# Kernel optimization log

Measured on AMD Instinct MI355X. Metric: run time of the kernel, lower is better.

The kernel has to match this reference:

```python
import jax, jax.numpy as jnp
import numpy as np

B, N, D = 1, 128, 64
H, DH = 8, 64            # heads, per-head dim; dim_inner = dim*dim_head = 512
DI = H * DH              # 512
L = 2                    # max_degree
S = 1 + 2 * L            # 5 degree slots: (h, r_1..L, x_1..L)
MLP = 1024               # int(2.0 * dim_inner)
EPS = 1e-5


def _ln(x, g):
    m = x.mean(-1, keepdims=True)
    v = ((x - m) ** 2).mean(-1, keepdims=True)
    return (x - m) * jax.lax.rsqrt(v + EPS) * g


def setup_inputs() -> dict:
    key = jax.random.key(0)
    ks = jax.random.split(key, 16)
    rn = lambda k, s, sc=1.0: jax.random.normal(k, s, dtype=jnp.float32) * sc
    return {
        "h": rn(ks[0], (B, N, D)),
        "t_ij": rn(ks[1], (B, N, N, D)),
        "r1": rn(ks[2], (B, N, N, 3)),
        "r2": rn(ks[3], (B, N, N, 5)),
        "x1": rn(ks[4], (B, N, D, 3)),
        "x2": rn(ks[5], (B, N, D, 5)),
        "g_hi": jnp.ones((D,), jnp.float32),
        "g_hj": jnp.ones((D,), jnp.float32),
        "Wq": rn(ks[6], (D, DI), D ** -0.5),
        "Wk": rn(ks[7], (D, DI), D ** -0.5),
        "Wv1": rn(ks[8], (D, MLP), D ** -0.5),
        "bv1": jnp.zeros((MLP,), jnp.float32),
        "Wv2": rn(ks[9], (MLP, S * DI), MLP ** -0.5),
        "bv2": jnp.zeros((S * DI,), jnp.float32),
        "Wp1": rn(ks[10], (D, MLP), D ** -0.5),
        "bp1": jnp.zeros((MLP,), jnp.float32),
        "Wp2": rn(ks[11], (MLP, S * DI), MLP ** -0.5),
        "bp2": jnp.zeros((S * DI,), jnp.float32),
        "Wev": rn(ks[12], (D, S * DI), D ** -0.5),
        "Wc": rn(ks[13], (DI, D), DI ** -0.5),
    }


def reference(h, t_ij, r1, r2, x1, x2, g_hi, g_hj, Wq, Wk, Wv1, bv1, Wv2, bv2,
              Wp1, bp1, Wp2, bp2, Wev, Wc):
    b, n, d = h.shape
    hi, hj = _ln(h, g_hi), _ln(h, g_hj)
    q = (hi @ Wq).reshape(b, n, H, DH).transpose(0, 2, 1, 3)                # b h i d
    k = (hj @ Wk).reshape(b, n, H, DH).transpose(0, 2, 1, 3)                # b h j d
    vals = (jax.nn.silu(hj @ Wv1 + bv1) @ Wv2 + bv2)
    vals = vals.reshape(b, n, S, H, DH).transpose(0, 3, 1, 2, 4)            # b h j s d
    pav = (jax.nn.silu(hj @ Wp1 + bp1) @ Wp2 + bp2)
    pav = pav.reshape(b, n, S, H, DH).transpose(0, 3, 1, 2, 4)              # b h j s d
    # NOTE: source uses to_edge_values for BOTH edge keys and edge values (to_edge_keys is dead code)
    ev = (t_ij @ Wev).reshape(b, n, n, S, H, DH).transpose(0, 4, 1, 2, 3, 5)  # b h i j s d
    sim_num = jnp.einsum('bhid,bhjd->bhij', q, k)                           # b h i j
    sim_den = jnp.einsum('bhid,bhijsd->bhis', q, ev)                        # b h i s
    attn = sim_num[..., None] / sim_den[:, :, :, None, :]                   # b h i j s (quotient attention)
    sea = attn[..., None] * vals[:, :, None] + ev * pav[:, :, None]         # b h i j s d
    out = sea.transpose(0, 2, 3, 4, 1, 5).reshape(b, n, n, S, DI) @ Wc      # b i j s D
    # split sizes (1, L, L) along the s axis: h scale, r_ij scales, x scales
    h_new = h + out[:, :, :, 0, :].sum(axis=2)                              # sum over neighbors j
    xs, rs = (x1, x2), (r1, r2)
    x_new = [jnp.einsum('bjdm,bijd->bidm', xs[l], out[:, :, :, 1 + L + l, :])
             + jnp.einsum('bijm,bijd->bidm', rs[l], out[:, :, :, 1 + l, :])
             for l in range(L)]
    return (h_new, x_new[0], x_new[1])
```

## Files before the change

### kernel.cpp

```cpp
#include <hip/hip_runtime.h>
#include <hip/hip_bf16.h>

typedef __hip_bfloat16 bf16;
typedef __attribute__((ext_vector_type(8))) short short8;
typedef __attribute__((ext_vector_type(4))) float f32x4;

#define NN 128
#define DD_ 64
#define HH_ 8
#define DH_ 64
#define DI_ 512
#define SS_ 5
#define MLPD 1024
#define SDI 2560

__device__ __forceinline__ float wave_sum64(float v) {
#pragma unroll
    for (int off = 32; off > 0; off >>= 1) v += __shfl_xor(v, off, 64);
    return v;
}

__device__ __forceinline__ unsigned short f2bf_u(float f) {
    unsigned u = __float_as_uint(f);
    u += 0x7FFF + ((u >> 16) & 1);
    return (unsigned short)(u >> 16);
}
__device__ __forceinline__ float bfu2f(unsigned short s) {
    return __uint_as_float(((unsigned)s) << 16);
}
__device__ __forceinline__ unsigned pk2(unsigned short a, unsigned short b) {
    return (unsigned)a | ((unsigned)b << 16);
}

__global__ __launch_bounds__(256) void k_front(
    const float* __restrict__ h, const float* __restrict__ ghi, const float* __restrict__ ghj,
    const float* __restrict__ Wq, const float* __restrict__ Wk,
    const float* __restrict__ Wv1, const float* __restrict__ bv1,
    const float* __restrict__ Wp1, const float* __restrict__ bp1,
    float* __restrict__ q, float* __restrict__ k,
    float* __restrict__ a1, float* __restrict__ p1) {
    int i = blockIdx.x, ch = blockIdx.y, t = threadIdx.x;
    int d = t & 63;
    __shared__ float hib[DD_], hjb[DD_];
    float x = h[i * DD_ + d];
    float s = wave_sum64(x);
    float s2 = wave_sum64(x * x);
    float m = s * (1.0f / DD_);
    float v = s2 * (1.0f / DD_) - m * m;
    float r = rsqrtf(v + 1e-5f);
    float xc = (x - m) * r;
    if (t < 64) { hib[d] = xc * ghi[d]; hjb[d] = xc * ghj[d]; }
    __syncthreads();
    {
        int c = ch * 128 + (t & 127);
        const float* W = (t < 128) ? Wq : Wk;
        const float* hb = (t < 128) ? hib : hjb;
        float a = 0.f;
#pragma unroll 8
        for (int dd = 0; dd < DD_; dd++) a += hb[dd] * W[dd * DI_ + c];
        float* dstqk = (t < 128) ? q : k;
        dstqk[i * DI_ + c] = a;
    }
    {
        int c = ch * 256 + t;
        float av = 0.f, ap = 0.f;
#pragma unroll 4
        for (int dd = 0; dd < DD_; dd++) {
            float hv = hjb[dd];
            av += hv * Wv1[dd * MLPD + c];
            ap += hv * Wp1[dd * MLPD + c];
        }
        float xv = av + bv1[c], xp = ap + bp1[c];
        a1[i * MLPD + c] = xv / (1.0f + expf(-xv));
        p1[i * MLPD + c] = xp / (1.0f + expf(-xp));
    }
}

#define KSP 8
#define KSL 128
__global__ __launch_bounds__(256) void k_mlp2(const float* __restrict__ a1,
                                              const float* __restrict__ p1,
                                              const float* __restrict__ Wv2,
                                              const float* __restrict__ Wp2,
                                              float* __restrict__ part) {
    int ct = blockIdx.x, ks = blockIdx.y, t = threadIdx.x;
    int c0 = ct * 128;
    bool isp = c0 >= 2560;
    int c0l = c0 - (isp ? 2560 : 0);
    const float* __restrict__ src = isp ? p1 : a1;
    const float* __restrict__ W = isp ? Wp2 : Wv2;
    int k0base = ks * KSL;
    __shared__ float As[128][33];
    __shared__ float Ws[32][128];
    int tc = t & 7;
    int tj = t >> 3;
    int j0 = tj * 4;
    float acc[4][16];
#pragma unroll
    for (int jj = 0; jj < 4; jj++)
#pragma unroll
        for (int cc = 0; cc < 16; cc++) acc[jj][cc] = 0.f;
    for (int kc = 0; kc < KSL; kc += 32) {
        int k0 = k0base + kc;
        __syncthreads();
#pragma unroll
        for (int it = 0; it < 4; it++) {
            int slot = t + it * 256;
            int jj = slot >> 3, f4 = (slot & 7) * 4;
            float4 v = *(const float4*)&src[jj * MLPD + k0 + f4];
            As[jj][f4 + 0] = v.x; As[jj][f4 + 1] = v.y;
            As[jj][f4 + 2] = v.z; As[jj][f4 + 3] = v.w;
        }
#pragma unroll
        for (int it = 0; it < 4; it++) {
            int slot = t + it * 256;
            int kk = slot >> 5, f4 = (slot & 31) * 4;
            float4 v = *(const float4*)&W[(size_t)(k0 + kk) * SDI + c0l + f4];
            *(float4*)&Ws[kk][f4] = v;
        }
        __syncthreads();
#pragma unroll 4
        for (int kx = 0; kx < 32; kx++) {
            float a[4];
#pragma unroll
            for (int jj = 0; jj < 4; jj++) a[jj] = As[j0 + jj][kx];
#pragma unroll
            for (int cf = 0; cf < 4; cf++) {
                float4 wv = *(const float4*)&Ws[kx][tc * 4 + cf * 32];
#pragma unroll
                for (int jj = 0; jj < 4; jj++) {
                    acc[jj][cf * 4 + 0] += a[jj] * wv.x;
                    acc[jj][cf * 4 + 1] += a[jj] * wv.y;
                    acc[jj][cf * 4 + 2] += a[jj] * wv.z;
                    acc[jj][cf * 4 + 3] += a[jj] * wv.w;
                }
            }
        }
    }
#pragma unroll
    for (int jj = 0; jj < 4; jj++)
#pragma unroll
        for (int cf = 0; cf < 4; cf++) {
            float4 v = make_float4(acc[jj][cf * 4 + 0], acc[jj][cf * 4 + 1],
                                   acc[jj][cf * 4 + 2], acc[jj][cf * 4 + 3]);
            *(float4*)&part[(size_t)ks * 655360 + (size_t)(j0 + jj) * 5120 + c0 + tc * 4 + cf * 32] = v;
        }
}

__global__ __launch_bounds__(512) void k_post(const float* __restrict__ part,
                                              const float* __restrict__ bv2,
                                              const float* __restrict__ bp2,
                                              const float* __restrict__ Wc,
                                              float* __restrict__ pav,
                                              float* __restrict__ VC) {
    int j = blockIdx.x, y = blockIdx.y, t = threadIdx.x;
    if (y < 5) {
        int s = y;
        __shared__ float vlds[512];
        int e = s * 512 + t;
        float sum = 0.f;
#pragma unroll
        for (int p = 0; p < KSP; p++) sum += part[(size_t)p * 655360 + (size_t)j * 5120 + e];
        vlds[t] = sum + bv2[e];
        __syncthreads();
        int dd = t & 63;
        int hbase = t - dd;
        float acc = 0.f;
#pragma unroll 8
        for (int d2 = 0; d2 < DH_; d2++) acc += vlds[hbase + d2] * Wc[(size_t)(hbase + d2) * DD_ + dd];
        VC[(size_t)(j * SS_ + s) * DI_ + t] = acc;
    } else {
        int s = y - 5;
        int e = 2560 + s * 512 + t;
        float sum = 0.f;
#pragma unroll
        for (int p = 0; p < KSP; p++) sum += part[(size_t)p * 655360 + (size_t)j * 5120 + e];
        pav[(size_t)j * SDI + s * 512 + t] = sum + bp2[s * 512 + t];
    }
}

__global__ __launch_bounds__(640) void k_den(const float* __restrict__ tij,
                                             const float* __restrict__ Wev,
                                             const float* __restrict__ q,
                                             float* __restrict__ rsd) {
    int i = blockIdx.x, half = blockIdx.y, t = threadIdx.x;
    __shared__ float red[10][64];
    __shared__ float Tl[64];
    __shared__ float ql[DI_];
    int c = t & 63, jw = t >> 6;
    float s = 0.f;
    for (int j = jw; j < NN; j += 10) s += tij[(size_t)(i * NN + j) * DD_ + c];
    red[jw][c] = s;
    if (t < DI_) ql[t] = q[i * DI_ + t];
    __syncthreads();
    if (t < 64) {
        float a = 0.f;
#pragma unroll
        for (int r2 = 0; r2 < 10; r2++) a += red[r2][t];
        Tl[t] = a;
    }
    __syncthreads();
#pragma unroll
    for (int kx = 0; kx < 2; kx++) {
        int u = half * 1280 + kx * 640 + t;
        float ev = 0.f;
#pragma unroll 8
        for (int cc = 0; cc < DD_; cc++) ev += Tl[cc] * Wev[(size_t)cc * SDI + u];
        float den = wave_sum64(ev * ql[u & 511]);
        if ((t & 63) == 0) {
            int g = u >> 6;
            int ss = g >> 3, hh = g & 7;
            rsd[i * 40 + hh * SS_ + ss] = 1.0f / den;
        }
    }
}

__global__ __launch_bounds__(512) void k_simnum(const float* __restrict__ q,
                                                const float* __restrict__ k,
                                                float* __restrict__ sn) {
    int i = blockIdx.x, yh = blockIdx.y, t = threadIdx.x;
    int hh = yh * 4 + (t >> 7), j = t & 127;
    __shared__ float qb[256];
    if (t < 256) qb[t] = q[i * DI_ + yh * 256 + t];
    __syncthreads();
    float a = 0.f;
    const float* kr = &k[(size_t)j * DI_ + hh * DH_];
    const float* qr = &qb[(hh - yh * 4) * DH_];
#pragma unroll 8
    for (int d = 0; d < DH_; d++) a += qr[d] * kr[d];
    sn[i * 1024 + hh * NN + j] = a;
}

#define KCM 64
__global__ __launch_bounds__(256) void k_M(const float* __restrict__ pav,
                                           const float* __restrict__ Wev,
                                           const float* __restrict__ Wc,
                                           float* __restrict__ M) {
    int j = blockIdx.x, s = blockIdx.y, t = threadIdx.x;
    int lane = t & 63, w = t >> 6;
    __shared__ float P[DI_];
    __shared__ unsigned short Ahi[64][72], Alo[64][72];
    __shared__ unsigned short Bhi[64][72], Blo[64][72];
    P[t] = pav[j * SDI + s * DI_ + t];
    P[t + 256] = pav[j * SDI + s * DI_ + t + 256];
    f32x4 acc[4];
#pragma unroll
    for (int n = 0; n < 4; n++) acc[n] = (f32x4){0.f, 0.f, 0.f, 0.f};
    __syncthreads();
    for (int u0 = 0; u0 < DI_; u0 += KCM) {
        {
            int c = t >> 2, ug = (t & 3) * 16;
            const float* wevp = &Wev[(size_t)c * SDI + s * DI_ + u0 + ug];
            unsigned short ah[16], al[16];
#pragma unroll
            for (int e = 0; e < 16; e += 4) {
                float4 wv = *(const float4*)(wevp + e);
                float4 pv = *(const float4*)&P[u0 + ug + e];
                float av[4] = {wv.x * pv.x, wv.y * pv.y, wv.z * pv.z, wv.w * pv.w};
#pragma unroll
                for (int z = 0; z < 4; z++) {
                    unsigned short hh2 = f2bf_u(av[z]);
                    ah[e + z] = hh2;
                    al[e + z] = f2bf_u(av[z] - bfu2f(hh2));
                }
            }
            *(uint4*)&Ahi[c][ug] = make_uint4(pk2(ah[0], ah[1]), pk2(ah[2], ah[3]),
                                              pk2(ah[4], ah[5]), pk2(ah[6], ah[7]));
            *(uint4*)&Ahi[c][ug + 8] = make_uint4(pk2(ah[8], ah[9]), pk2(ah[10], ah[11]),
                                                  pk2(ah[12], ah[13]), pk2(ah[14], ah[15]));
            *(uint4*)&Alo[c][ug] = make_uint4(pk2(al[0], al[1]), pk2(al[2], al[3]),
                                              pk2(al[4], al[5]), pk2(al[6], al[7]));
            *(uint4*)&Alo[c][ug + 8] = make_uint4(pk2(al[8], al[9]), pk2(al[10], al[11]),
                                                  pk2(al[12], al[13]), pk2(al[14], al[15]));
        }
        {
            int dd = t & 63, ub = (t >> 6) * 16;
            unsigned short bh[16], bl[16];
#pragma unroll
            for (int e = 0; e < 16; e++) {
                float v = Wc[(size_t)(u0 + ub + e) * DD_ + dd];
                unsigned short hh2 = f2bf_u(v);
                bh[e] = hh2;
                bl[e] = f2bf_u(v - bfu2f(hh2));
            }
            *(uint4*)&Bhi[dd][ub] = make_uint4(pk2(bh[0], bh[1]), pk2(bh[2], bh[3]),
                                               pk2(bh[4], bh[5]), pk2(bh[6], bh[7]));
            *(uint4*)&Bhi[dd][ub + 8] = make_uint4(pk2(bh[8], bh[9]), pk2(bh[10], bh[11]),
                                                   pk2(bh[12], bh[13]), pk2(bh[14], bh[15]));
            *(uint4*)&Blo[dd][ub] = make_uint4(pk2(bl[0], bl[1]), pk2(bl[2], bl[3]),
                                               pk2(bl[4], bl[5]), pk2(bl[6], bl[7]));
            *(uint4*)&Blo[dd][ub + 8] = make_uint4(pk2(bl[8], bl[9]), pk2(bl[10], bl[11]),
                                                   pk2(bl[12], bl[13]), pk2(bl[14], bl[15]));
        }
        __syncthreads();
#pragma unroll
        for (int kk = 0; kk < 2; kk++) {
            int ko = kk * 32 + (lane >> 4) * 8;
            short8 a_h = *(const short8*)&Ahi[w * 16 + (lane & 15)][ko];
            short8 a_l = *(const short8*)&Alo[w * 16 + (lane & 15)][ko];
#pragma unroll
            for (int n = 0; n < 4; n++) {
                short8 b_h = *(const short8*)&Bhi[n * 16 + (lane & 15)][ko];
                short8 b_l = *(const short8*)&Blo[n * 16 + (lane & 15)][ko];
                acc[n] = __builtin_amdgcn_mfma_f32_16x16x32_bf16(a_h, b_h, acc[n], 0, 0, 0);
                acc[n] = __builtin_amdgcn_mfma_f32_16x16x32_bf16(a_h, b_l, acc[n], 0, 0, 0);
                acc[n] = __builtin_amdgcn_mfma_f32_16x16x32_bf16(a_l, b_h, acc[n], 0, 0, 0);
            }
        }
        __syncthreads();
    }
    float* Mp = &M[(size_t)(j * SS_ + s) * 4096];
#pragma unroll
    for (int n = 0; n < 4; n++)
#pragma unroll
        for (int r = 0; r < 4; r++) {
            int c = w * 16 + (lane >> 4) * 4 + r;
            int dd = n * 16 + (lane & 15);
            Mp[c * 64 + dd] = acc[n][r];
        }
}

__global__ __launch_bounds__(256) void k_out(const float* __restrict__ M, const float* __restrict__ VC,
                      const float* __restrict__ sn, const float* __restrict__ rsd,
                      const float* __restrict__ tij, float* __restrict__ outb) {
    int j = blockIdx.x, s = blockIdx.y, ic = blockIdx.z, t = threadIdx.x;
    int il = t >> 6, dd = t & 63;
    __shared__ float VCl[DI_];
    __shared__ float tl[4][64];
    __shared__ float snl[4][8];
    __shared__ float rl[4][8];
    float Mcol[64];
    const float* Mp = &M[(size_t)(j * SS_ + s) * 4096];
#pragma unroll
    for (int c = 0; c < 64; c++) Mcol[c] = Mp[c * 64 + dd];
    VCl[t] = VC[(j * SS_ + s) * DI_ + t];
    VCl[t + 256] = VC[(j * SS_ + s) * DI_ + t + 256];
    __syncthreads();
    for (int ib = ic * 64; ib < ic * 64 + 64; ib += 4) {
        int i = ib + il;
        tl[il][dd] = tij[(size_t)(i * NN + j) * DD_ + dd];
        if (dd < 8) {
            snl[il][dd] = sn[i * 1024 + dd * NN + j];
            rl[il][dd] = rsd[i * 40 + dd * SS_ + s];
        }
        float A = 0.f;
#pragma unroll
        for (int hh = 0; hh < HH_; hh++) A += snl[il][hh] * rl[il][hh] * VCl[hh * DH_ + dd];
        float E = 0.f;
        const float4* tl4 = (const float4*)&tl[il][0];
#pragma unroll
        for (int c4 = 0; c4 < 16; c4++) {
            float4 tv = tl4[c4];
            E += tv.x * Mcol[4 * c4] + tv.y * Mcol[4 * c4 + 1] +
                 tv.z * Mcol[4 * c4 + 2] + tv.w * Mcol[4 * c4 + 3];
        }
        outb[((size_t)(i * NN + j) * SS_ + s) * 64 + dd] = A + E;
    }
}

#define JC 16
#define JPC 8
__global__ void k_red1(const float* __restrict__ outb,
                       const float* __restrict__ r1, const float* __restrict__ r2,
                       const float* __restrict__ x1, const float* __restrict__ x2,
                       float* __restrict__ pr) {
    int i = blockIdx.x, jc = blockIdx.y, t = threadIdx.x;
    int s = t >> 6, dd = t & 63;
    int jbeg = jc * JPC;
    float hacc = 0.f;
    float am[5] = {0.f, 0.f, 0.f, 0.f, 0.f};
    for (int jj = 0; jj < JPC; jj++) {
        int j = jbeg + jj;
        float ov = outb[((size_t)(i * NN + j) * SS_ + s) * 64 + dd];
        if (s == 0) {
            hacc += ov;
        } else if (s == 1) {
#pragma unroll
            for (int m = 0; m < 3; m++) am[m] += r1[(i * NN + j) * 3 + m] * ov;
        } else if (s == 2) {
#pragma unroll
            for (int m = 0; m < 5; m++) am[m] += r2[(i * NN + j) * 5 + m] * ov;
        } else if (s == 3) {
#pragma unroll
            for (int m = 0; m < 3; m++) am[m] += x1[(j * DD_ + dd) * 3 + m] * ov;
        } else {
#pragma unroll
            for (int m = 0; m < 5; m++) am[m] += x2[(j * DD_ + dd) * 5 + m] * ov;
        }
    }
    float* rec = &pr[(size_t)(i * JC + jc) * 1088];
    if (s == 0) {
        rec[dd] = hacc;
    } else if (s == 1) {
#pragma unroll
        for (int m = 0; m < 3; m++) rec[64 + dd * 3 + m] = am[m];
    } else if (s == 2) {
#pragma unroll
        for (int m = 0; m < 5; m++) rec[256 + dd * 5 + m] = am[m];
    } else if (s == 3) {
#pragma unroll
        for (int m = 0; m < 3; m++) rec[576 + dd * 3 + m] = am[m];
    } else {
#pragma unroll
        for (int m = 0; m < 5; m++) rec[768 + dd * 5 + m] = am[m];
    }
}

__global__ void k_red2(const float* __restrict__ pr, const float* __restrict__ h,
                       float* __restrict__ dst) {
    int i = blockIdx.x, t = threadIdx.x;
    int s = t >> 6, dd = t & 63;
    const float* base = &pr[(size_t)i * JC * 1088];
    if (s == 0) {
        float v = 0.f;
#pragma unroll
        for (int c = 0; c < JC; c++) v += base[c * 1088 + dd];
        dst[i * DD_ + dd] = h[i * DD_ + dd] + v;
    } else if (s == 3) {
        float v[3] = {0.f, 0.f, 0.f};
#pragma unroll
        for (int c = 0; c < JC; c++) {
#pragma unroll
            for (int m = 0; m < 3; m++)
                v[m] += base[c * 1088 + 64 + dd * 3 + m] + base[c * 1088 + 576 + dd * 3 + m];
        }
#pragma unroll
        for (int m = 0; m < 3; m++)
            dst[8192 + (i * DD_ + dd) * 3 + m] = v[m];
    } else if (s == 4) {
        float v[5] = {0.f, 0.f, 0.f, 0.f, 0.f};
#pragma unroll
        for (int c = 0; c < JC; c++) {
#pragma unroll
            for (int m = 0; m < 5; m++)
                v[m] += base[c * 1088 + 256 + dd * 5 + m] + base[c * 1088 + 768 + dd * 5 + m];
        }
#pragma unroll
        for (int m = 0; m < 5; m++)
            dst[8192 + 24576 + (i * DD_ + dd) * 5 + m] = v[m];
    }
}

extern "C" void kernel_launch(void* const* d_in, const int* in_sizes, int n_in,
                              void* d_out, int out_size, void* d_ws, size_t ws_size,
                              hipStream_t stream) {
    const float* h_in = (const float*)d_in[0];
    const float* tij = (const float*)d_in[1];
    const float* r1 = (const float*)d_in[2];
    const float* r2 = (const float*)d_in[3];
    const float* x1 = (const float*)d_in[4];
    const float* x2 = (const float*)d_in[5];
    const float* ghi = (const float*)d_in[6];
    const float* ghj = (const float*)d_in[7];
    const float* Wq = (const float*)d_in[8];
    const float* Wk = (const float*)d_in[9];
    const float* Wv1 = (const float*)d_in[10];
    const float* bv1 = (const float*)d_in[11];
    const float* Wv2 = (const float*)d_in[12];
    const float* bv2 = (const float*)d_in[13];
    const float* Wp1 = (const float*)d_in[14];
    const float* bp1 = (const float*)d_in[15];
    const float* Wp2 = (const float*)d_in[16];
    const float* bp2 = (const float*)d_in[17];
    const float* Wev = (const float*)d_in[18];
    const float* Wc = (const float*)d_in[19];
    float* dst = (float*)d_out;

    float* w = (float*)d_ws;
    size_t off = 16;
    auto alloc = [&](size_t n) { float* p = w + off; off += n; return p; };
    float* q    = alloc(65536);
    float* k    = alloc(65536);
    float* a1   = alloc(131072);
    float* p1   = alloc(131072);
    float* pav  = alloc(327680);
    float* VC   = alloc(327680);
    float* sn   = alloc(131072);
    float* rsd  = alloc(5120);
    float* M    = alloc(2621440);
    float* outb = alloc(5242880);
    float* part = alloc(5242880);
    float* pr   = alloc(2228224);

    k_front<<<dim3(128, 4), dim3(256), 0, stream>>>(h_in, ghi, ghj, Wq, Wk, Wv1, bv1, Wp1, bp1,
                                                    q, k, a1, p1);
    k_mlp2<<<dim3(40, KSP), dim3(256), 0, stream>>>(a1, p1, Wv2, Wp2, part);
    k_post<<<dim3(128, 10), dim3(512), 0, stream>>>(part, bv2, bp2, Wc, pav, VC);
    k_den<<<dim3(128, 2), dim3(640), 0, stream>>>(tij, Wev, q, rsd);
    k_simnum<<<dim3(128, 2), dim3(512), 0, stream>>>(q, k, sn);
    k_M<<<dim3(128, 5), dim3(256), 0, stream>>>(pav, Wev, Wc, M);
    k_out<<<dim3(128, 5, 2), dim3(256), 0, stream>>>(M, VC, sn, rsd, tij, outb);
    k_red1<<<dim3(128, JC), dim3(320), 0, stream>>>(outb, r1, r2, x1, x2, pr);
    k_red2<<<dim3(128), dim3(320), 0, stream>>>(pr, h_in, dst);
}
```

Measured before the change: 244.4 us.

## Move MLP2 and k_out GEMMs onto split-bf16 MFMA

Rewrites k_mlp2 to use bf16 hi/lo split MFMA (three products per tile) instead of scalar FP32 FMAs. The tile changes to 64 columns and the K split to 4, which halves the partial buffer. k_out becomes a 128x64 MFMA GEMM per (j,s) block: the sn·rsd·VC term is folded in as a zero-padded K=8 chunk and the tij·M product as two K=32 chunks. This removes scalar FMA throughput limits, at the cost of converting to bf16 pairs on the fly and dropping the low×low product, which loses a little accuracy.

```diff
diff --git a/kernel.cpp b/kernel.cpp
--- a/kernel.cpp
+++ b/kernel.cpp
@@ -76,75 +76,98 @@
     }
 }
 
-#define KSP 8
-#define KSL 128
+#define KS2 4
 __global__ __launch_bounds__(256) void k_mlp2(const float* __restrict__ a1,
                                               const float* __restrict__ p1,
                                               const float* __restrict__ Wv2,
                                               const float* __restrict__ Wp2,
                                               float* __restrict__ part) {
     int ct = blockIdx.x, ks = blockIdx.y, t = threadIdx.x;
-    int c0 = ct * 128;
+    int c0 = ct * 64;
     bool isp = c0 >= 2560;
     int c0l = c0 - (isp ? 2560 : 0);
     const float* __restrict__ src = isp ? p1 : a1;
     const float* __restrict__ W = isp ? Wp2 : Wv2;
-    int k0base = ks * KSL;
-    __shared__ float As[128][33];
-    __shared__ float Ws[32][128];
-    int tc = t & 7;
-    int tj = t >> 3;
-    int j0 = tj * 4;
-    float acc[4][16];
-#pragma unroll
-    for (int jj = 0; jj < 4; jj++)
-#pragma unroll
-        for (int cc = 0; cc < 16; cc++) acc[jj][cc] = 0.f;
-    for (int kc = 0; kc < KSL; kc += 32) {
-        int k0 = k0base + kc;
+    int kbase = ks * 256;
+    __shared__ unsigned short Ahi[128][40], Alo[128][40];
+    __shared__ unsigned short Bhi[64][40], Blo[64][40];
+    int lane = t & 63, wv = t >> 6;
+    int l15 = lane & 15, quad = lane >> 4;
+    f32x4 acc[2][4];
+#pragma unroll
+    for (int mt = 0; mt < 2; mt++)
+#pragma unroll
+        for (int nt = 0; nt < 4; nt++) acc[mt][nt] = (f32x4){0.f, 0.f, 0.f, 0.f};
+    int aj = t >> 1, ak = (t & 1) * 16;
+    int bc = t & 63, bk = (t >> 6) * 8;
+    for (int kc = 0; kc < 8; kc++) {
+        int k0 = kbase + kc * 32;
         __syncthreads();
-#pragma unroll
-        for (int it = 0; it < 4; it++) {
-            int slot = t + it * 256;
-            int jj = slot >> 3, f4 = (slot & 7) * 4;
-            float4 v = *(const float4*)&src[jj * MLPD + k0 + f4];
-            As[jj][f4 + 0] = v.x; As[jj][f4 + 1] = v.y;
-            As[jj][f4 + 2] = v.z; As[jj][f4 + 3] = v.w;
-        }
-#pragma unroll
-        for (int it = 0; it < 4; it++) {
-            int slot = t + it * 256;
-            int kk = slot >> 5, f4 = (slot & 31) * 4;
-            float4 v = *(const float4*)&W[(size_t)(k0 + kk) * SDI + c0l + f4];
-            *(float4*)&Ws[kk][f4] = v;
+        {
+            unsigned short h16[16], l16[16];
+            const float* ap = &src[(size_t)aj * MLPD + k0 + ak];
+#pragma unroll
+            for (int e = 0; e < 16; e += 4) {
+                float4 v = *(const float4*)(ap + e);
+                float vv[4] = {v.x, v.y, v.z, v.w};
+#pragma unroll
+                for (int z = 0; z < 4; z++) {
+                    unsigned short hb = f2bf_u(vv[z]);
+                    h16[e + z] = hb;
+                    l16[e + z] = f2bf_u(vv[z] - bfu2f(hb));
+                }
+            }
+            *(uint4*)&Ahi[aj][ak] = make_uint4(pk2(h16[0], h16[1]), pk2(h16[2], h16[3]),
+                                               pk2(h16[4], h16[5]), pk2(h16[6], h16[7]));
+            *(uint4*)&Ahi[aj][ak + 8] = make_uint4(pk2(h16[8], h16[9]), pk2(h16[10], h16[11]),
+                                                   pk2(h16[12], h16[13]), pk2(h16[14], h16[15]));
+            *(uint4*)&Alo[aj][ak] = make_uint4(pk2(l16[0], l16[1]), pk2(l16[2], l16[3]),
+                                               pk2(l16[4], l16[5]), pk2(l16[6], l16[7]));
+            *(uint4*)&Alo[aj][ak + 8] = make_uint4(pk2(l16[8], l16[9]), pk2(l16[10], l16[11]),
+                                                   pk2(l16[12], l16[13]), pk2(l16[14], l16[15]));
+        }
+        {
+            unsigned short h8[8], l8[8];
+#pragma unroll
+            for (int e = 0; e < 8; e++) {
+                float v = W[(size_t)(k0 + bk + e) * SDI + c0l + bc];
+                unsigned short hb = f2bf_u(v);
+                h8[e] = hb;
+                l8[e] = f2bf_u(v - bfu2f(hb));
+            }
+            *(uint4*)&Bhi[bc][bk] = make_uint4(pk2(h8[0], h8[1]), pk2(h8[2], h8[3]),
+                                               pk2(h8[4], h8[5]), pk2(h8[6], h8[7]));
+            *(uint4*)&Blo[bc][bk] = make_uint4(pk2(l8[0], l8[1]), pk2(l8[2], l8[3]),
+                                               pk2(l8[4], l8[5]), pk2(l8[6], l8[7]));
         }
         __syncthreads();
-#pragma unroll 4
-        for (int kx = 0; kx < 32; kx++) {
-            float a[4];
-#pragma unroll
-            for (int jj = 0; jj < 4; jj++) a[jj] = As[j0 + jj][kx];
-#pragma unroll
-            for (int cf = 0; cf < 4; cf++) {
-                float4 wv = *(const float4*)&Ws[kx][tc * 4 + cf * 32];
-#pragma unroll
-                for (int jj = 0; jj < 4; jj++) {
-                    acc[jj][cf * 4 + 0] += a[jj] * wv.x;
-                    acc[jj][cf * 4 + 1] += a[jj] * wv.y;
-                    acc[jj][cf * 4 + 2] += a[jj] * wv.z;
-                    acc[jj][cf * 4 + 3] += a[jj] * wv.w;
-                }
-            }
-        }
-    }
-#pragma unroll
-    for (int jj = 0; jj < 4; jj++)
-#pragma unroll
-        for (int cf = 0; cf < 4; cf++) {
-            float4 v = make_float4(acc[jj][cf * 4 + 0], acc[jj][cf * 4 + 1],
-                                   acc[jj][cf * 4 + 2], acc[jj][cf * 4 + 3]);
-            *(float4*)&part[(size_t)ks * 655360 + (size_t)(j0 + jj) * 5120 + c0 + tc * 4 + cf * 32] = v;
-        }
+        int ko = quad * 8;
+        short8 a_h0 = *(const short8*)&Ahi[(wv * 2 + 0) * 16 + l15][ko];
+        short8 a_l0 = *(const short8*)&Alo[(wv * 2 + 0) * 16 + l15][ko];
+        short8 a_h1 = *(const short8*)&Ahi[(wv * 2 + 1) * 16 + l15][ko];
+        short8 a_l1 = *(const short8*)&Alo[(wv * 2 + 1) * 16 + l15][ko];
+#pragma unroll
+        for (int nt = 0; nt < 4; nt++) {
+            short8 b_h = *(const short8*)&Bhi[nt * 16 + l15][ko];
+            short8 b_l = *(const short8*)&Blo[nt * 16 + l15][ko];
+            acc[0][nt] = __builtin_amdgcn_mfma_f32_16x16x32_bf16(a_h0, b_h, acc[0][nt], 0, 0, 0);
+            acc[0][nt] = __builtin_amdgcn_mfma_f32_16x16x32_bf16(a_h0, b_l, acc[0][nt], 0, 0, 0);
+            acc[0][nt] = __builtin_amdgcn_mfma_f32_16x16x32_bf16(a_l0, b_h, acc[0][nt], 0, 0, 0);
+            acc[1][nt] = __builtin_amdgcn_mfma_f32_16x16x32_bf16(a_h1, b_h, acc[1][nt], 0, 0, 0);
+            acc[1][nt] = __builtin_amdgcn_mfma_f32_16x16x32_bf16(a_h1, b_l, acc[1][nt], 0, 0, 0);
+            acc[1][nt] = __builtin_amdgcn_mfma_f32_16x16x32_bf16(a_l1, b_h, acc[1][nt], 0, 0, 0);
+        }
+    }
+#pragma unroll
+    for (int mt = 0; mt < 2; mt++)
+#pragma unroll
+        for (int nt = 0; nt < 4; nt++)
+#pragma unroll
+            for (int r = 0; r < 4; r++) {
+                int j = (wv * 2 + mt) * 16 + quad * 4 + r;
+                int cc = c0 + nt * 16 + l15;
+                part[(size_t)ks * 655360 + (size_t)j * 5120 + cc] = acc[mt][nt][r];
+            }
 }
 
 __global__ __launch_bounds__(512) void k_post(const float* __restrict__ part,
@@ -160,7 +183,7 @@
         int e = s * 512 + t;
         float sum = 0.f;
 #pragma unroll
-        for (int p = 0; p < KSP; p++) sum += part[(size_t)p * 655360 + (size_t)j * 5120 + e];
+        for (int p = 0; p < KS2; p++) sum += part[(size_t)p * 655360 + (size_t)j * 5120 + e];
         vlds[t] = sum + bv2[e];
         __syncthreads();
         int dd = t & 63;
@@ -174,7 +197,7 @@
         int e = 2560 + s * 512 + t;
         float sum = 0.f;
 #pragma unroll
-        for (int p = 0; p < KSP; p++) sum += part[(size_t)p * 655360 + (size_t)j * 5120 + e];
+        for (int p = 0; p < KS2; p++) sum += part[(size_t)p * 655360 + (size_t)j * 5120 + e];
         pav[(size_t)j * SDI + s * 512 + t] = sum + bp2[s * 512 + t];
     }
 }
@@ -321,41 +344,147 @@
 }
 
 __global__ __launch_bounds__(256) void k_out(const float* __restrict__ M, const float* __restrict__ VC,
-                      const float* __restrict__ sn, const float* __restrict__ rsd,
-                      const float* __restrict__ tij, float* __restrict__ outb) {
-    int j = blockIdx.x, s = blockIdx.y, ic = blockIdx.z, t = threadIdx.x;
-    int il = t >> 6, dd = t & 63;
-    __shared__ float VCl[DI_];
-    __shared__ float tl[4][64];
-    __shared__ float snl[4][8];
-    __shared__ float rl[4][8];
-    float Mcol[64];
-    const float* Mp = &M[(size_t)(j * SS_ + s) * 4096];
-#pragma unroll
-    for (int c = 0; c < 64; c++) Mcol[c] = Mp[c * 64 + dd];
-    VCl[t] = VC[(j * SS_ + s) * DI_ + t];
-    VCl[t + 256] = VC[(j * SS_ + s) * DI_ + t + 256];
+                                             const float* __restrict__ sn, const float* __restrict__ rsd,
+                                             const float* __restrict__ tij, float* __restrict__ outb) {
+    int j = blockIdx.x, s = blockIdx.y, t = threadIdx.x;
+    int lane = t & 63, wv = t >> 6, l15 = lane & 15, quad = lane >> 4;
+    __shared__ unsigned short Ahi[128][40], Alo[128][40];
+    __shared__ unsigned short Bhi[64][40], Blo[64][40];
+    f32x4 acc[2][4];
+#pragma unroll
+    for (int mt = 0; mt < 2; mt++)
+#pragma unroll
+        for (int nt = 0; nt < 4; nt++) acc[mt][nt] = (f32x4){0.f, 0.f, 0.f, 0.f};
+    {
+        int i = t >> 1, hg = (t & 1) * 4;
+        unsigned short h4[4], l4[4];
+#pragma unroll
+        for (int e = 0; e < 4; e++) {
+            int hh_ = hg + e;
+            float v = sn[i * 1024 + hh_ * NN + j] * rsd[i * 40 + hh_ * SS_ + s];
+            unsigned short hb = f2bf_u(v);
+            h4[e] = hb;
+            l4[e] = f2bf_u(v - bfu2f(hb));
+        }
+        *(uint2*)&Ahi[i][hg] = make_uint2(pk2(h4[0], h4[1]), pk2(h4[2], h4[3]));
+        *(uint2*)&Alo[i][hg] = make_uint2(pk2(l4[0], l4[1]), pk2(l4[2], l4[3]));
+#pragma unroll
+        for (int r = 0; r < 2; r++) {
+            int idx = t + r * 256;
+            if (idx < 384) {
+                int ii = idx / 3, g = idx % 3;
+                *(uint4*)&Ahi[ii][8 + g * 8] = make_uint4(0, 0, 0, 0);
+                *(uint4*)&Alo[ii][8 + g * 8] = make_uint4(0, 0, 0, 0);
+            }
+        }
+        if (t < 64) {
+            unsigned short h8[8], l8[8];
+#pragma unroll
+            for (int e = 0; e < 8; e++) {
+                float v = VC[(size_t)(j * SS_ + s) * DI_ + e * 64 + t];
+                unsigned short hb = f2bf_u(v);
+                h8[e] = hb;
+                l8[e] = f2bf_u(v - bfu2f(hb));
+            }
+            *(uint4*)&Bhi[t][0] = make_uint4(pk2(h8[0], h8[1]), pk2(h8[2], h8[3]),
+                                             pk2(h8[4], h8[5]), pk2(h8[6], h8[7]));
+            *(uint4*)&Blo[t][0] = make_uint4(pk2(l8[0], l8[1]), pk2(l8[2], l8[3]),
+                                             pk2(l8[4], l8[5]), pk2(l8[6], l8[7]));
+        } else {
+            int idx = t - 64;
+            int dd2 = idx / 3, g = idx % 3;
+            *(uint4*)&Bhi[dd2][8 + g * 8] = make_uint4(0, 0, 0, 0);
+            *(uint4*)&Blo[dd2][8 + g * 8] = make_uint4(0, 0, 0, 0);
+        }
+    }
     __syncthreads();
-    for (int ib = ic * 64; ib < ic * 64 + 64; ib += 4) {
-        int i = ib + il;
-        tl[il][dd] = tij[(size_t)(i * NN + j) * DD_ + dd];
-        if (dd < 8) {
-            snl[il][dd] = sn[i * 1024 + dd * NN + j];
-            rl[il][dd] = rsd[i * 40 + dd * SS_ + s];
-        }
-        float A = 0.f;
-#pragma unroll
-        for (int hh = 0; hh < HH_; hh++) A += snl[il][hh] * rl[il][hh] * VCl[hh * DH_ + dd];
-        float E = 0.f;
-        const float4* tl4 = (const float4*)&tl[il][0];
-#pragma unroll
-        for (int c4 = 0; c4 < 16; c4++) {
-            float4 tv = tl4[c4];
-            E += tv.x * Mcol[4 * c4] + tv.y * Mcol[4 * c4 + 1] +
-                 tv.z * Mcol[4 * c4 + 2] + tv.w * Mcol[4 * c4 + 3];
-        }
-        outb[((size_t)(i * NN + j) * SS_ + s) * 64 + dd] = A + E;
-    }
+    {
+        int ko = quad * 8;
+        short8 a_h0 = *(const short8*)&Ahi[(wv * 2 + 0) * 16 + l15][ko];
+        short8 a_l0 = *(const short8*)&Alo[(wv * 2 + 0) * 16 + l15][ko];
+        short8 a_h1 = *(const short8*)&Ahi[(wv * 2 + 1) * 16 + l15][ko];
+        short8 a_l1 = *(const short8*)&Alo[(wv * 2 + 1) * 16 + l15][ko];
+#pragma unroll
+        for (int nt = 0; nt < 4; nt++) {
+            short8 b_h = *(const short8*)&Bhi[nt * 16 + l15][ko];
+            short8 b_l = *(const short8*)&Blo[nt * 16 + l15][ko];
+            acc[0][nt] = __builtin_amdgcn_mfma_f32_16x16x32_bf16(a_h0, b_h, acc[0][nt], 0, 0, 0);
+            acc[0][nt] = __builtin_amdgcn_mfma_f32_16x16x32_bf16(a_h0, b_l, acc[0][nt], 0, 0, 0);
+            acc[0][nt] = __builtin_amdgcn_mfma_f32_16x16x32_bf16(a_l0, b_h, acc[0][nt], 0, 0, 0);
+            acc[1][nt] = __builtin_amdgcn_mfma_f32_16x16x32_bf16(a_h1, b_h, acc[1][nt], 0, 0, 0);
+            acc[1][nt] = __builtin_amdgcn_mfma_f32_16x16x32_bf16(a_h1, b_l, acc[1][nt], 0, 0, 0);
+            acc[1][nt] = __builtin_amdgcn_mfma_f32_16x16x32_bf16(a_l1, b_h, acc[1][nt], 0, 0, 0);
+        }
+    }
+    for (int kc = 0; kc < 2; kc++) {
+        __syncthreads();
+        {
+            int i = t >> 1, chalf = (t & 1) * 16;
+            unsigned short h16[16], l16[16];
+            const float* tp = &tij[(size_t)(i * NN + j) * DD_ + kc * 32 + chalf];
+#pragma unroll
+            for (int e = 0; e < 16; e += 4) {
+                float4 v = *(const float4*)(tp + e);
+                float vv[4] = {v.x, v.y, v.z, v.w};
+#pragma unroll
+                for (int z = 0; z < 4; z++) {
+                    unsigned short hb = f2bf_u(vv[z]);
+                    h16[e + z] = hb;
+                    l16[e + z] = f2bf_u(vv[z] - bfu2f(hb));
+                }
+            }
+            *(uint4*)&Ahi[i][chalf] = make_uint4(pk2(h16[0], h16[1]), pk2(h16[2], h16[3]),
+                                                 pk2(h16[4], h16[5]), pk2(h16[6], h16[7]));
+            *(uint4*)&Ahi[i][chalf + 8] = make_uint4(pk2(h16[8], h16[9]), pk2(h16[10], h16[11]),
+                                                     pk2(h16[12], h16[13]), pk2(h16[14], h16[15]));
+            *(uint4*)&Alo[i][chalf] = make_uint4(pk2(l16[0], l16[1]), pk2(l16[2], l16[3]),
+                                                 pk2(l16[4], l16[5]), pk2(l16[6], l16[7]));
+            *(uint4*)&Alo[i][chalf + 8] = make_uint4(pk2(l16[8], l16[9]), pk2(l16[10], l16[11]),
+                                                     pk2(l16[12], l16[13]), pk2(l16[14], l16[15]));
+        }
+        {
+            int dd2 = t & 63, cg = (t >> 6) * 8;
+            unsigned short h8[8], l8[8];
+#pragma unroll
+            for (int e = 0; e < 8; e++) {
+                float v = M[(size_t)(j * SS_ + s) * 4096 + (size_t)(kc * 32 + cg + e) * 64 + dd2];
+                unsigned short hb = f2bf_u(v);
+                h8[e] = hb;
+                l8[e] = f2bf_u(v - bfu2f(hb));
+            }
+            *(uint4*)&Bhi[dd2][cg] = make_uint4(pk2(h8[0], h8[1]), pk2(h8[2], h8[3]),
+                                                pk2(h8[4], h8[5]), pk2(h8[6], h8[7]));
+            *(uint4*)&Blo[dd2][cg] = make_uint4(pk2(l8[0], l8[1]), pk2(l8[2], l8[3]),
+                                                pk2(l8[4], l8[5]), pk2(l8[6], l8[7]));
+        }
+        __syncthreads();
+        int ko = quad * 8;
+        short8 a_h0 = *(const short8*)&Ahi[(wv * 2 + 0) * 16 + l15][ko];
+        short8 a_l0 = *(const short8*)&Alo[(wv * 2 + 0) * 16 + l15][ko];
+        short8 a_h1 = *(const short8*)&Ahi[(wv * 2 + 1) * 16 + l15][ko];
+        short8 a_l1 = *(const short8*)&Alo[(wv * 2 + 1) * 16 + l15][ko];
+#pragma unroll
+        for (int nt = 0; nt < 4; nt++) {
+            short8 b_h = *(const short8*)&Bhi[nt * 16 + l15][ko];
+            short8 b_l = *(const short8*)&Blo[nt * 16 + l15][ko];
+            acc[0][nt] = __builtin_amdgcn_mfma_f32_16x16x32_bf16(a_h0, b_h, acc[0][nt], 0, 0, 0);
+            acc[0][nt] = __builtin_amdgcn_mfma_f32_16x16x32_bf16(a_h0, b_l, acc[0][nt], 0, 0, 0);
+            acc[0][nt] = __builtin_amdgcn_mfma_f32_16x16x32_bf16(a_l0, b_h, acc[0][nt], 0, 0, 0);
+            acc[1][nt] = __builtin_amdgcn_mfma_f32_16x16x32_bf16(a_h1, b_h, acc[1][nt], 0, 0, 0);
+            acc[1][nt] = __builtin_amdgcn_mfma_f32_16x16x32_bf16(a_h1, b_l, acc[1][nt], 0, 0, 0);
+            acc[1][nt] = __builtin_amdgcn_mfma_f32_16x16x32_bf16(a_l1, b_h, acc[1][nt], 0, 0, 0);
+        }
+    }
+#pragma unroll
+    for (int mt = 0; mt < 2; mt++)
+#pragma unroll
+        for (int nt = 0; nt < 4; nt++)
+#pragma unroll
+            for (int r = 0; r < 4; r++) {
+                int i = (wv * 2 + mt) * 16 + quad * 4 + r;
+                int dd = nt * 16 + l15;
+                outb[((size_t)(i * NN + j) * SS_ + s) * 64 + dd] = acc[mt][nt][r];
+            }
 }
 
 #define JC 16
@@ -479,17 +608,17 @@
     float* rsd  = alloc(5120);
     float* M    = alloc(2621440);
     float* outb = alloc(5242880);
-    float* part = alloc(5242880);
+    float* part = alloc(2621440);
     float* pr   = alloc(2228224);
 
     k_front<<<dim3(128, 4), dim3(256), 0, stream>>>(h_in, ghi, ghj, Wq, Wk, Wv1, bv1, Wp1, bp1,
                                                     q, k, a1, p1);
-    k_mlp2<<<dim3(40, KSP), dim3(256), 0, stream>>>(a1, p1, Wv2, Wp2, part);
+    k_mlp2<<<dim3(80, KS2), dim3(256), 0, stream>>>(a1, p1, Wv2, Wp2, part);
     k_post<<<dim3(128, 10), dim3(512), 0, stream>>>(part, bv2, bp2, Wc, pav, VC);
     k_den<<<dim3(128, 2), dim3(640), 0, stream>>>(tij, Wev, q, rsd);
     k_simnum<<<dim3(128, 2), dim3(512), 0, stream>>>(q, k, sn);
     k_M<<<dim3(128, 5), dim3(256), 0, stream>>>(pav, Wev, Wc, M);
-    k_out<<<dim3(128, 5, 2), dim3(256), 0, stream>>>(M, VC, sn, rsd, tij, outb);
+    k_out<<<dim3(128, 5), dim3(256), 0, stream>>>(M, VC, sn, rsd, tij, outb);
     k_red1<<<dim3(128, JC), dim3(320), 0, stream>>>(outb, r1, r2, x1, x2, pr);
     k_red2<<<dim3(128), dim3(320), 0, stream>>>(pr, h_in, dst);
 }
```

Measured after the change: 203.9 us. 16.6% less time.
